# Performance work log

Hardware: AMD Instinct MI355X
Metric: run time of the kernel (lower is better)

## Reference

```python
import jax, jax.numpy as jnp
import numpy as np

NUM_HEADS = 32
NUM_KV = 8
Q_MULT = NUM_HEADS // NUM_KV  # 4
HEAD_DIM = 128
WINDOW = 1024
SM_SCALE = 1.0 / np.sqrt(HEAD_DIM)


def setup_inputs() -> dict:
    key = jax.random.key(0)
    k1, k2, k3, k4 = jax.random.split(key, 4)
    B, S = 2, 2048
    Q = jax.random.normal(k1, (B, S, NUM_HEADS * HEAD_DIM), dtype=jnp.float32)
    K = jax.random.normal(k2, (B, S, NUM_KV * HEAD_DIM), dtype=jnp.float32)
    V = jax.random.normal(k3, (B, S, NUM_KV * HEAD_DIM), dtype=jnp.float32)
    sinks = jax.random.normal(k4, (NUM_HEADS,), dtype=jnp.float32) * 0.1
    return {"Q": Q, "K": K, "V": V, "sinks": sinks}


def reference(Q, K, V, sinks):
    B, S, _ = Q.shape
    # GQA layout: head = kv * q_mult + m (matches Q[b].view(S, kv, q_mult, d))
    Qh = Q.reshape(B, S, NUM_KV, Q_MULT, HEAD_DIM)
    Kh = K.reshape(B, S, NUM_KV, HEAD_DIM)
    Vh = V.reshape(B, S, NUM_KV, HEAD_DIM)

    # scores: [B, kv, q_mult, S_q, S_k]
    scores = jnp.einsum('bqhmd,bkhd->bhmqk', Qh, Kh) * SM_SCALE

    q_idx = jnp.arange(S)[:, None]
    k_idx = jnp.arange(S)[None, :]
    # causal AND within sliding window: q - WINDOW < k <= q
    allowed = (k_idx <= q_idx) & (k_idx > q_idx - WINDOW)
    scores = jnp.where(allowed[None, None, None, :, :], scores, -jnp.inf)

    # learned sink logit per head, appended as an extra softmax column
    sink = sinks.reshape(NUM_KV, Q_MULT)[None, :, :, None, None]
    sink = jnp.broadcast_to(sink, (B, NUM_KV, Q_MULT, S, 1))
    logits = jnp.concatenate([scores, sink], axis=-1)
    w = jax.nn.softmax(logits, axis=-1)[..., :-1]  # drop sink column

    out = jnp.einsum('bhmqk,bkhd->bqhmd', w, Vh)
    return out.reshape(B, S, NUM_HEADS * HEAD_DIM)
```

## Files before the change

kernel.cpp:

```cpp
#include <hip/hip_runtime.h>
#include <stdint.h>

#define S_LEN 2048
#define HD    128
#define NKV   8
#define NQM   4
#define WIN   1024
#define QB    32
#define KTILE 32
#define KVROW (NKV * HD)
#define QROW  (NQM * NKV * HD)

typedef __attribute__((ext_vector_type(8))) short bf16x8;
typedef __attribute__((ext_vector_type(4))) float f32x4;
typedef __attribute__((ext_vector_type(4))) int   i32x4;

__device__ __forceinline__ uint32_t f2bf(float f) {
  uint32_t x = __builtin_bit_cast(uint32_t, f);
  x += 0x7fffu + ((x >> 16) & 1u);
  return x >> 16;
}

__device__ __forceinline__ uint32_t cvtpk(float lo, float hi) {
  uint32_t r;
  asm("v_cvt_pk_bf16_f32 %0, %1, %2" : "=v"(r) : "v"(lo), "v"(hi));
  return r;
}
__device__ __forceinline__ uint32_t perm2(uint32_t a, uint32_t b, uint32_t sel) {
  uint32_t r;
  asm("v_perm_b32 %0, %1, %2, %3" : "=v"(r) : "v"(a), "v"(b), "s"(sel));
  return r;
}

__device__ __forceinline__ void load8bf(const uint16_t* p, uint32_t o[4]) {
  i32x4 v = *reinterpret_cast<const i32x4*>(p);
  o[0] = (uint32_t)v[0]; o[1] = (uint32_t)v[1]; o[2] = (uint32_t)v[2]; o[3] = (uint32_t)v[3];
}
__device__ __forceinline__ void load8bf(const float* p, uint32_t o[4]) {
  float4 a = *reinterpret_cast<const float4*>(p);
  float4 b = *reinterpret_cast<const float4*>(p + 4);
  o[0] = cvtpk(a.x, a.y);
  o[1] = cvtpk(a.z, a.w);
  o[2] = cvtpk(b.x, b.y);
  o[3] = cvtpk(b.z, b.w);
}

__global__ void cvt2_kernel(const float* __restrict__ inK, const float* __restrict__ inV,
                            uint16_t* __restrict__ outK, uint16_t* __restrict__ outV, int n4) {
  int i = blockIdx.x * blockDim.x + threadIdx.x;
  int stride = gridDim.x * blockDim.x;
  for (int j = i; j < 2 * n4; j += stride) {
    const float* in = (j < n4) ? inK : inV;
    uint16_t* out   = (j < n4) ? outK : outV;
    int jj = (j < n4) ? j : j - n4;
    float4 v = reinterpret_cast<const float4*>(in)[jj];
    uint2 o;
    o.x = cvtpk(v.x, v.y);
    o.y = cvtpk(v.z, v.w);
    reinterpret_cast<uint2*>(out)[jj] = o;
  }
}

#define VSWZ(d) (((((uint32_t)(d) >> 3) ^ (uint32_t)(d)) & 7u) << 3)

template <typename KVT>
__launch_bounds__(256, 2)
__global__ void attn_kernel(const float* __restrict__ Q,
                            const KVT* __restrict__ Ksrc,
                            const KVT* __restrict__ Vsrc,
                            const float* __restrict__ sinks,
                            float* __restrict__ out) {
  __shared__ __align__(16) uint8_t smem[40960];

  const int tid  = threadIdx.x;
  const int lane = tid & 63;
  const int wv   = tid >> 6;
  const int c    = lane & 15;
  const int g    = lane >> 4;
  uint8_t* pls = smem + 32768 + wv * 2048;

  const int bid = blockIdx.x;
  const int kv  = bid & 7;
  const int i2  = bid >> 3;
  const int b   = i2 / 48;
  const int pairIdx = i2 % 48;
  const int head = kv * NQM + wv;
  const float sink_l2 = sinks[head] * 1.4426950408889634f;

  int qtA, qtB, nrep;
  if (pairIdx < 16) { qtA = 31 - pairIdx; qtB = pairIdx; nrep = 2; }
  else              { qtA = pairIdx + 16; qtB = 0;       nrep = 1; }

  const int kr  = tid >> 3;
  const int kcB = (tid & 7) * 32;
  const uint32_t kw0 = (uint32_t)(kr * 256 + ((kcB)      ^ ((kr & 7) << 4)));
  const uint32_t kw1 = (uint32_t)(kr * 256 + ((kcB + 16) ^ ((kr & 7) << 4)));
  const KVT* kg = Ksrc + (size_t)(b * S_LEN) * KVROW + kv * HD + (tid & 7) * 16;
  const size_t kbase = (size_t)(b * S_LEN) * KVROW + kv * HD;
  const int va = tid >> 4;
  const int vd = tid & 15;
  const KVT* vg = Vsrc + (size_t)(b * S_LEN) * KVROW + kv * HD + vd * 8;

  uint32_t vr0[4], vr1[4];

  auto stageK = [&](uint8_t* kbuf, int kt) {
    if constexpr (sizeof(KVT) == 2) {
      #pragma unroll
      for (int ch = 0; ch < 2; ++ch) {
        const int o    = wv * 2048 + ch * 1024 + lane * 16;
        const int row  = o >> 8;
        const int scol = (o & 255) ^ ((row & 7) << 4);
        const uint8_t* gp = (const uint8_t*)(Ksrc + kbase + (size_t)(kt + row) * KVROW) + scol;
        __builtin_amdgcn_global_load_lds(
            (const __attribute__((address_space(1))) void*)gp,
            (__attribute__((address_space(3))) void*)(kbuf + wv * 2048 + ch * 1024),
            16, 0, 0);
      }
    } else {
      const KVT* src = kg + (size_t)(kt + kr) * KVROW;
      uint32_t t0[4], t1[4];
      load8bf(src, t0); load8bf(src + 8, t1);
      i32x4 w0, w1;
      w0[0]=(int)t0[0]; w0[1]=(int)t0[1]; w0[2]=(int)t0[2]; w0[3]=(int)t0[3];
      w1[0]=(int)t1[0]; w1[1]=(int)t1[1]; w1[2]=(int)t1[2]; w1[3]=(int)t1[3];
      *reinterpret_cast<i32x4*>(kbuf + kw0) = w0;
      *reinterpret_cast<i32x4*>(kbuf + kw1) = w1;
    }
  };
  auto loadV = [&](int kt) {
    const KVT* vs = vg + (size_t)(kt + 2 * va) * KVROW;
    load8bf(vs, vr0); load8bf(vs + KVROW, vr1);
  };
  auto writeV = [&](uint8_t* vbuf) {
    #pragma unroll
    for (int ii = 0; ii < 8; ++ii) {
      int d = vd * 8 + ii;
      uint32_t w = (ii & 1) ? perm2(vr1[ii >> 1], vr0[ii >> 1], 0x07060302u)
                            : perm2(vr1[ii >> 1], vr0[ii >> 1], 0x05040100u);
      uint32_t byte = (uint32_t)(d * 64) + (((uint32_t)(va * 4)) ^ VSWZ(d));
      *reinterpret_cast<uint32_t*>(vbuf + byte) = w;
    }
  };

  const float SCALE2 = 0.08838834764831845f * 1.4426950408889634f;
  const uint32_t sp = ((uint32_t)(c & 7)) << 3;

  for (int rep = 0; rep < nrep; ++rep) {
    const int q0 = (rep ? qtB : qtA) * QB;

    bf16x8 qf[2][4];
    #pragma unroll
    for (int tq = 0; tq < 2; ++tq) {
      const float* qp = Q + (size_t)(b * S_LEN + q0 + tq * 16 + c) * QROW + head * HD;
      #pragma unroll
      for (int f = 0; f < 4; ++f) {
        int d0 = f * 32 + g * 8;
        float4 a = *reinterpret_cast<const float4*>(qp + d0);
        float4 bb = *reinterpret_cast<const float4*>(qp + d0 + 4);
        i32x4 t;
        t[0] = (int)cvtpk(a.x * SCALE2, a.y * SCALE2);
        t[1] = (int)cvtpk(a.z * SCALE2, a.w * SCALE2);
        t[2] = (int)cvtpk(bb.x * SCALE2, bb.y * SCALE2);
        t[3] = (int)cvtpk(bb.z * SCALE2, bb.w * SCALE2);
        qf[tq][f] = __builtin_bit_cast(bf16x8, t);
      }
    }

    float m_[2] = {sink_l2, sink_l2};
    float lp_[2] = {0.25f, 0.25f};
    f32x4 acc[2][8];
    #pragma unroll
    for (int tq = 0; tq < 2; ++tq)
      #pragma unroll
      for (int dt = 0; dt < 8; ++dt) acc[tq][dt] = (f32x4)0.0f;

    int kstart = q0 - (WIN - 1);
    if (kstart < 0) kstart = 0;
    kstart &= ~(KTILE - 1);

    uint8_t* kcur = smem;         uint8_t* kalt = smem + 8192;
    uint8_t* vcur = smem + 16384; uint8_t* valt = smem + 24576;

    loadV(kstart);
    stageK(kcur, kstart);
    writeV(vcur);
    __syncthreads();

    for (int kt = kstart; kt <= q0; kt += KTILE) {
      const bool more = (kt + KTILE) <= q0;
      if (more) {
        stageK(kalt, kt + KTILE);
        loadV(kt + KTILE);
      }

      f32x4 st[2][2];
      #pragma unroll
      for (int a_ = 0; a_ < 2; ++a_)
        #pragma unroll
        for (int b_ = 0; b_ < 2; ++b_) st[a_][b_] = (f32x4)0.0f;

      __builtin_amdgcn_s_setprio(1);
      #pragma unroll
      for (int kt_ = 0; kt_ < 2; ++kt_) {
        bf16x8 kf[4];
        #pragma unroll
        for (int f = 0; f < 4; ++f) {
          int row = kt_ * 16 + c;
          uint32_t byte = (uint32_t)(row * 256 + ((f * 64 + g * 16) ^ ((row & 7) << 4)));
          kf[f] = *reinterpret_cast<const bf16x8*>(kcur + byte);
        }
        #pragma unroll
        for (int tq = 0; tq < 2; ++tq)
          #pragma unroll
          for (int f = 0; f < 4; ++f)
            st[kt_][tq] = __builtin_amdgcn_mfma_f32_16x16x32_bf16(kf[f], qf[tq][f], st[kt_][tq], 0, 0, 0);
      }
      __builtin_amdgcn_s_setprio(0);

      const bool need_mask = (kt + KTILE - 1 > q0) || (kt < q0 + QB - WIN);
      if (need_mask) {
        #pragma unroll
        for (int kt_ = 0; kt_ < 2; ++kt_)
          #pragma unroll
          for (int tq = 0; tq < 2; ++tq)
            #pragma unroll
            for (int r = 0; r < 4; ++r) {
              int k_ = kt + kt_ * 16 + g * 4 + r;
              int q_ = q0 + tq * 16 + c;
              bool ok = (k_ <= q_) && (k_ > q_ - WIN);
              if (!ok) st[kt_][tq][r] = -1e38f;
            }
      }

      #pragma unroll
      for (int tq = 0; tq < 2; ++tq) {
        float ownmax = fmaxf(fmaxf(fmaxf(st[0][tq][0], st[0][tq][1]), fmaxf(st[0][tq][2], st[0][tq][3])),
                             fmaxf(fmaxf(st[1][tq][0], st[1][tq][1]), fmaxf(st[1][tq][2], st[1][tq][3])));
        const float mold = m_[tq];
        if (!__all(ownmax <= mold + 11.54f)) {
          float vmax = fmaxf(ownmax, __shfl_xor(ownmax, 16));
          vmax = fmaxf(vmax, __shfl_xor(vmax, 32));
          float mnew = fmaxf(mold, vmax);
          float scl  = exp2f(mold - mnew);
          m_[tq] = mnew;
          lp_[tq] *= scl;
          float sc[4];
          #pragma unroll
          for (int r = 0; r < 4; ++r) sc[r] = __shfl(scl, (lane & 48) | (g * 4 + r));
          #pragma unroll
          for (int dt = 0; dt < 8; ++dt)
            #pragma unroll
            for (int r = 0; r < 4; ++r) acc[tq][dt][r] *= sc[r];
        }
        const float mrun = m_[tq];
        float p[2][4];
        float s = 0.0f;
        #pragma unroll
        for (int kt_ = 0; kt_ < 2; ++kt_)
          #pragma unroll
          for (int r = 0; r < 4; ++r) {
            float e = exp2f(st[kt_][tq][r] - mrun);
            p[kt_][r] = e;
            s += e;
          }
        lp_[tq] += s;
        #pragma unroll
        for (int kt_ = 0; kt_ < 2; ++kt_) {
          uint2 pk;
          pk.x = cvtpk(p[kt_][0], p[kt_][1]);
          pk.y = cvtpk(p[kt_][2], p[kt_][3]);
          uint32_t byte = (uint32_t)((tq * 16 + c) * 64) + (((uint32_t)(kt_ * 32 + g * 8)) ^ sp);
          *reinterpret_cast<uint2*>(pls + byte) = pk;
        }
      }

      bf16x8 pa[2];
      #pragma unroll
      for (int tq = 0; tq < 2; ++tq) {
        uint32_t base = (uint32_t)((tq * 16 + c) * 64);
        uint2 plo = *reinterpret_cast<const uint2*>(pls + base + (((uint32_t)(g * 16))     ^ sp));
        uint2 phi = *reinterpret_cast<const uint2*>(pls + base + (((uint32_t)(g * 16 + 8)) ^ sp));
        i32x4 pv; pv[0] = (int)plo.x; pv[1] = (int)plo.y; pv[2] = (int)phi.x; pv[3] = (int)phi.y;
        pa[tq] = __builtin_bit_cast(bf16x8, pv);
      }
      __builtin_amdgcn_s_setprio(1);
      #pragma unroll
      for (int dt = 0; dt < 8; ++dt) {
        int d = dt * 16 + c;
        uint32_t rowb = (uint32_t)(d * 64);
        uint32_t swz  = VSWZ(d);
        uint2 lo = *reinterpret_cast<const uint2*>(vcur + rowb + (((uint32_t)(g * 16))     ^ swz));
        uint2 hi = *reinterpret_cast<const uint2*>(vcur + rowb + (((uint32_t)(g * 16 + 8)) ^ swz));
        i32x4 vv; vv[0] = (int)lo.x; vv[1] = (int)lo.y; vv[2] = (int)hi.x; vv[3] = (int)hi.y;
        bf16x8 vf = __builtin_bit_cast(bf16x8, vv);
        #pragma unroll
        for (int tq = 0; tq < 2; ++tq)
          acc[tq][dt] = __builtin_amdgcn_mfma_f32_16x16x32_bf16(pa[tq], vf, acc[tq][dt], 0, 0, 0);
      }
      __builtin_amdgcn_s_setprio(0);

      if (more) writeV(valt);
      __syncthreads();
      uint8_t* t0 = kcur; kcur = kalt; kalt = t0;
      uint8_t* t1 = vcur; vcur = valt; valt = t1;
    }

    #pragma unroll
    for (int tq = 0; tq < 2; ++tq) {
      float lt = lp_[tq];
      lt += __shfl_xor(lt, 16);
      lt += __shfl_xor(lt, 32);
      float linv = 1.0f / lt;
      float li[4];
      #pragma unroll
      for (int r = 0; r < 4; ++r) li[r] = __shfl(linv, (lane & 48) | (g * 4 + r));
      #pragma unroll
      for (int dt = 0; dt < 8; ++dt)
        #pragma unroll
        for (int r = 0; r < 4; ++r) {
          size_t o = (size_t)(b * S_LEN + q0 + tq * 16 + g * 4 + r) * QROW + head * HD + dt * 16 + c;
          out[o] = acc[tq][dt][r] * li[r];
        }
    }
  }
}

extern "C" void kernel_launch(void* const* d_in, const int* in_sizes, int n_in,
                              void* d_out, int out_size, void* d_ws, size_t ws_size,
                              hipStream_t stream) {
  const float* Q     = (const float*)d_in[0];
  const float* K     = (const float*)d_in[1];
  const float* V     = (const float*)d_in[2];
  const float* sinks = (const float*)d_in[3];
  float* out = (float*)d_out;

  const int nK = in_sizes[1];
  const int B  = in_sizes[0] / (S_LEN * QROW);
  dim3 grid(384 * B);

  const size_t need = (size_t)nK * 2u * 2u;
  if (ws_size >= need) {
    uint16_t* Kb = (uint16_t*)d_ws;
    uint16_t* Vb = Kb + nK;
    cvt2_kernel<<<1024, 256, 0, stream>>>(K, V, Kb, Vb, nK / 4);
    attn_kernel<uint16_t><<<grid, 256, 0, stream>>>(Q, Kb, Vb, sinks, out);
  } else {
    attn_kernel<float><<<grid, 256, 0, stream>>>(Q, K, V, sinks, out);
  }
}
```

Baseline: 226.4 us.

## Permute K rows in LDS so P feeds PV MFMA directly from registers

Keys are written into shared memory in a permuted row order (KPERM/KPERMI), so the S accumulator layout from the QK MFMA already matches the A-operand layout needed by the PV MFMA. P is packed to bf16 in registers, which removes the per-wave shared-memory round trip and its scratch space. Shared memory drops from 40 KB to 32 KB and launch bounds are raised to 4 blocks per CU, which may force register spilling. The prefetch branch is also removed: on the last tile the current tile is reloaded redundantly.

```diff
diff --git a/kernel.cpp b/kernel.cpp
--- a/kernel.cpp
+++ b/kernel.cpp
@@ -14,12 +14,6 @@
 typedef __attribute__((ext_vector_type(8))) short bf16x8;
 typedef __attribute__((ext_vector_type(4))) float f32x4;
 typedef __attribute__((ext_vector_type(4))) int   i32x4;
-
-__device__ __forceinline__ uint32_t f2bf(float f) {
-  uint32_t x = __builtin_bit_cast(uint32_t, f);
-  x += 0x7fffu + ((x >> 16) & 1u);
-  return x >> 16;
-}
 
 __device__ __forceinline__ uint32_t cvtpk(float lo, float hi) {
   uint32_t r;
@@ -63,21 +57,23 @@
 
 #define VSWZ(d) (((((uint32_t)(d) >> 3) ^ (uint32_t)(d)) & 7u) << 3)
 
+#define KPERM(a)  ((((a) >> 2) & 3) * 8 + ((a) >> 4) * 4 + ((a) & 3))
+#define KPERMI(k) ((((k) >> 2) & 1) * 16 + ((k) >> 3) * 4 + ((k) & 3))
+
 template <typename KVT>
-__launch_bounds__(256, 2)
+__launch_bounds__(256, 4)
 __global__ void attn_kernel(const float* __restrict__ Q,
                             const KVT* __restrict__ Ksrc,
                             const KVT* __restrict__ Vsrc,
                             const float* __restrict__ sinks,
                             float* __restrict__ out) {
-  __shared__ __align__(16) uint8_t smem[40960];
+  __shared__ __align__(16) uint8_t smem[32768];
 
   const int tid  = threadIdx.x;
   const int lane = tid & 63;
   const int wv   = tid >> 6;
   const int c    = lane & 15;
   const int g    = lane >> 4;
-  uint8_t* pls = smem + 32768 + wv * 2048;
 
   const int bid = blockIdx.x;
   const int kv  = bid & 7;
@@ -91,28 +87,35 @@
   if (pairIdx < 16) { qtA = 31 - pairIdx; qtB = pairIdx; nrep = 2; }
   else              { qtA = pairIdx + 16; qtB = 0;       nrep = 1; }
 
+  const size_t kbase = (size_t)(b * S_LEN) * KVROW + kv * HD;
+  uint32_t kgo[2];
+  #pragma unroll
+  for (int ch = 0; ch < 2; ++ch) {
+    const int o    = wv * 2048 + ch * 1024 + lane * 16;
+    const int row  = o >> 8;
+    const int key  = KPERM(row);
+    const int scol = (o & 255) ^ ((row & 7) << 4);
+    kgo[ch] = (uint32_t)(key * (KVROW * 2) + scol);
+  }
   const int kr  = tid >> 3;
   const int kcB = (tid & 7) * 32;
-  const uint32_t kw0 = (uint32_t)(kr * 256 + ((kcB)      ^ ((kr & 7) << 4)));
-  const uint32_t kw1 = (uint32_t)(kr * 256 + ((kcB + 16) ^ ((kr & 7) << 4)));
-  const KVT* kg = Ksrc + (size_t)(b * S_LEN) * KVROW + kv * HD + (tid & 7) * 16;
-  const size_t kbase = (size_t)(b * S_LEN) * KVROW + kv * HD;
+  const int kpr = KPERMI(kr);
+  const uint32_t kw0 = (uint32_t)(kpr * 256 + ((kcB)      ^ ((kpr & 7) << 4)));
+  const uint32_t kw1 = (uint32_t)(kpr * 256 + ((kcB + 16) ^ ((kpr & 7) << 4)));
+  const KVT* kg = Ksrc + kbase + (tid & 7) * 16;
   const int va = tid >> 4;
   const int vd = tid & 15;
-  const KVT* vg = Vsrc + (size_t)(b * S_LEN) * KVROW + kv * HD + vd * 8;
+  const KVT* vg = Vsrc + kbase + vd * 8;
 
   uint32_t vr0[4], vr1[4];
 
   auto stageK = [&](uint8_t* kbuf, int kt) {
     if constexpr (sizeof(KVT) == 2) {
+      const uint8_t* kb = (const uint8_t*)(Ksrc + kbase) + (size_t)kt * (KVROW * 2);
       #pragma unroll
       for (int ch = 0; ch < 2; ++ch) {
-        const int o    = wv * 2048 + ch * 1024 + lane * 16;
-        const int row  = o >> 8;
-        const int scol = (o & 255) ^ ((row & 7) << 4);
-        const uint8_t* gp = (const uint8_t*)(Ksrc + kbase + (size_t)(kt + row) * KVROW) + scol;
         __builtin_amdgcn_global_load_lds(
-            (const __attribute__((address_space(1))) void*)gp,
+            (const __attribute__((address_space(1))) void*)(kb + kgo[ch]),
             (__attribute__((address_space(3))) void*)(kbuf + wv * 2048 + ch * 1024),
             16, 0, 0);
       }
@@ -143,7 +146,6 @@
   };
 
   const float SCALE2 = 0.08838834764831845f * 1.4426950408889634f;
-  const uint32_t sp = ((uint32_t)(c & 7)) << 3;
 
   for (int rep = 0; rep < nrep; ++rep) {
     const int q0 = (rep ? qtB : qtA) * QB;
@@ -187,11 +189,9 @@
     __syncthreads();
 
     for (int kt = kstart; kt <= q0; kt += KTILE) {
-      const bool more = (kt + KTILE) <= q0;
-      if (more) {
-        stageK(kalt, kt + KTILE);
-        loadV(kt + KTILE);
-      }
+      const int ktn = (kt + KTILE <= q0) ? (kt + KTILE) : kt;
+      stageK(kalt, ktn);
+      loadV(ktn);
 
       f32x4 st[2][2];
       #pragma unroll
@@ -225,13 +225,14 @@
           for (int tq = 0; tq < 2; ++tq)
             #pragma unroll
             for (int r = 0; r < 4; ++r) {
-              int k_ = kt + kt_ * 16 + g * 4 + r;
+              int k_ = kt + g * 8 + kt_ * 4 + r;
               int q_ = q0 + tq * 16 + c;
               bool ok = (k_ <= q_) && (k_ > q_ - WIN);
               if (!ok) st[kt_][tq][r] = -1e38f;
             }
       }
 
+      bf16x8 pa[2];
       #pragma unroll
       for (int tq = 0; tq < 2; ++tq) {
         float ownmax = fmaxf(fmaxf(fmaxf(st[0][tq][0], st[0][tq][1]), fmaxf(st[0][tq][2], st[0][tq][3])),
@@ -264,25 +265,14 @@
             s += e;
           }
         lp_[tq] += s;
-        #pragma unroll
-        for (int kt_ = 0; kt_ < 2; ++kt_) {
-          uint2 pk;
-          pk.x = cvtpk(p[kt_][0], p[kt_][1]);
-          pk.y = cvtpk(p[kt_][2], p[kt_][3]);
-          uint32_t byte = (uint32_t)((tq * 16 + c) * 64) + (((uint32_t)(kt_ * 32 + g * 8)) ^ sp);
-          *reinterpret_cast<uint2*>(pls + byte) = pk;
-        }
-      }
-
-      bf16x8 pa[2];
-      #pragma unroll
-      for (int tq = 0; tq < 2; ++tq) {
-        uint32_t base = (uint32_t)((tq * 16 + c) * 64);
-        uint2 plo = *reinterpret_cast<const uint2*>(pls + base + (((uint32_t)(g * 16))     ^ sp));
-        uint2 phi = *reinterpret_cast<const uint2*>(pls + base + (((uint32_t)(g * 16 + 8)) ^ sp));
-        i32x4 pv; pv[0] = (int)plo.x; pv[1] = (int)plo.y; pv[2] = (int)phi.x; pv[3] = (int)phi.y;
+        i32x4 pv;
+        pv[0] = (int)cvtpk(p[0][0], p[0][1]);
+        pv[1] = (int)cvtpk(p[0][2], p[0][3]);
+        pv[2] = (int)cvtpk(p[1][0], p[1][1]);
+        pv[3] = (int)cvtpk(p[1][2], p[1][3]);
         pa[tq] = __builtin_bit_cast(bf16x8, pv);
       }
+
       __builtin_amdgcn_s_setprio(1);
       #pragma unroll
       for (int dt = 0; dt < 8; ++dt) {
@@ -299,7 +289,7 @@
       }
       __builtin_amdgcn_s_setprio(0);
 
-      if (more) writeV(valt);
+      writeV(valt);
       __syncthreads();
       uint8_t* t0 = kcur; kcur = kalt; kalt = t0;
       uint8_t* t1 = vcur; vcur = valt; valt = t1;
```

New measurement: 551.3 us. 143% more time.
